# Kernel optimization log

Measured on AMD Instinct MI355X. Metric: run time of the kernel, lower is better.

The kernel has to match this reference:

```python
import jax, jax.numpy as jnp
import numpy as np

DIM = 1024
DFF = 4096
B, L = 4, 4096


def _lin_init(key, din, dout):
    k1, k2 = jax.random.split(key)
    bound = 1.0 / np.sqrt(din)
    w = jax.random.uniform(k1, (din, dout), jnp.float32, -bound, bound)
    b = jax.random.uniform(k2, (dout,), jnp.float32, -bound, bound)
    return w, b


def setup_inputs() -> dict:
    key = jax.random.key(0)
    ks = jax.random.split(key, 12)
    x = jax.random.normal(ks[0], (B, L, DIM), jnp.float32)
    hidden = jax.random.normal(ks[1], (B, DIM), jnp.float32)
    w_ln_z, b_ln_z = _lin_init(ks[2], DIM, DIM)
    w_dt, b_dt = _lin_init(ks[3], DIM, DIM)
    w_y, b_y = _lin_init(ks[4], DIM, DIM)
    w_yg, b_yg = _lin_init(ks[5], DIM, DIM)
    w_ff, b_ff = _lin_init(ks[6], DIM, DFF)
    w_ffg, b_ffg = _lin_init(ks[7], DIM, DFF)
    w_ffo, b_ffo = _lin_init(ks[8], DFF, DIM)
    g_sio = jnp.ones((DIM,), jnp.float32)
    g_ffn = jnp.ones((DIM,), jnp.float32)
    return dict(x=x, hidden=hidden, w_ln_z=w_ln_z, b_ln_z=b_ln_z, w_dt=w_dt,
                b_dt=b_dt, w_y=w_y, b_y=b_y, w_yg=w_yg, b_yg=b_yg,
                w_ff=w_ff, b_ff=b_ff, w_ffg=w_ffg, b_ffg=b_ffg,
                w_ffo=w_ffo, b_ffo=b_ffo, g_sio=g_sio, g_ffn=g_ffn)


def _rmsnorm(x, g, eps=1e-6):
    return x * jax.lax.rsqrt(jnp.mean(x * x, axis=-1, keepdims=True) + eps) * g


def reference(x, hidden, w_ln_z, b_ln_z, w_dt, b_dt, w_y, b_y, w_yg, b_yg,
              w_ff, b_ff, w_ffg, b_ffg, w_ffo, b_ffo, g_sio, g_ffn):
    silu = jax.nn.silu
    sp = jax.nn.softplus
    # --- SioConv branch ---
    residual = x
    xn = _rmsnorm(x, g_sio)
    dt = xn @ w_dt + b_dt
    ln_z = -sp(-(xn @ w_ln_z + b_ln_z))
    ln_da = -sp(-dt)           # log sigmoid(dt)
    ln_o_da = -sp(dt)          # log sigmoid(-dt)
    ln_o_da_cumsum = jnp.cumsum(ln_o_da, axis=1)
    lcse = jax.lax.cumlogsumexp(ln_z + ln_da - ln_o_da_cumsum, axis=1)
    h_inner = jnp.exp(lcse + ln_o_da_cumsum)                 # [B,L,D]
    h_cross = jnp.exp(ln_o_da_cumsum) * hidden[:, None, :]   # [B,L,D]
    h = h_inner + h_cross
    y = (h @ w_y + b_y) * silu(xn @ w_yg + b_yg)
    x = y + residual
    # --- FFN branch ---
    residual = x
    xn = _rmsnorm(x, g_ffn)
    ff = ((xn @ w_ff + b_ff) * silu(xn @ w_ffg + b_ffg)) @ w_ffo + b_ffo
    x = ff + residual
    return (x, h)
```

## Files before the change

kernel.cpp:

```cpp
#include <hip/hip_runtime.h>
#include <cstdint>
#include <cstddef>

using u16 = unsigned short;
using bf16x8 = __attribute__((ext_vector_type(8))) short;
using f32x4  = __attribute__((ext_vector_type(4))) float;

__device__ __forceinline__ u16 f2bf(float f) {
  unsigned u = __float_as_uint(f);
  u += 0x7fffu + ((u >> 16) & 1u);
  return (u16)(u >> 16);
}
__device__ __forceinline__ float bf2f(u16 h) {
  return __uint_as_float(((unsigned)h) << 16);
}

__device__ __forceinline__ void gload_lds16(const void* g, void* l) {
  auto gp = reinterpret_cast<const __attribute__((address_space(1))) char*>(
      reinterpret_cast<uintptr_t>(g));
  auto lp = reinterpret_cast<__attribute__((address_space(3))) char*>(
      reinterpret_cast<uintptr_t>(l));
  __builtin_amdgcn_global_load_lds(gp, lp, 16, 0, 0);
}

__global__ __launch_bounds__(256) void transpose_to_bf16(
    const float* __restrict__ W, u16* __restrict__ WT, int din, int dout) {
  __shared__ float tile[32][33];
  const int j0 = blockIdx.x * 32;
  const int i0 = blockIdx.y * 32;
  const int tx = threadIdx.x & 31;
  const int ty = threadIdx.x >> 5;
#pragma unroll
  for (int k = 0; k < 32; k += 8)
    tile[ty + k][tx] = W[(size_t)(i0 + ty + k) * dout + (j0 + tx)];
  __syncthreads();
#pragma unroll
  for (int k = 0; k < 32; k += 8)
    WT[(size_t)(j0 + ty + k) * din + (i0 + tx)] = f2bf(tile[tx][ty + k]);
}

__global__ __launch_bounds__(256) void rmsnorm_kernel(
    const float* __restrict__ x, const float* __restrict__ g, u16* __restrict__ xn) {
  const int row = blockIdx.x;
  const float4 v = ((const float4*)(x + (size_t)row * 1024))[threadIdx.x];
  float ss = v.x * v.x + v.y * v.y + v.z * v.z + v.w * v.w;
#pragma unroll
  for (int off = 32; off > 0; off >>= 1) ss += __shfl_down(ss, off, 64);
  __shared__ float red[4];
  if ((threadIdx.x & 63) == 0) red[threadIdx.x >> 6] = ss;
  __syncthreads();
  const float rs = rsqrtf((red[0] + red[1] + red[2] + red[3]) * (1.f / 1024.f) + 1e-6f);
  const float4 gv = ((const float4*)g)[threadIdx.x];
  ushort4 o;
  o.x = f2bf(v.x * rs * gv.x);
  o.y = f2bf(v.y * rs * gv.y);
  o.z = f2bf(v.z * rs * gv.z);
  o.w = f2bf(v.w * rs * gv.w);
  ((ushort4*)(xn + (size_t)row * 1024))[threadIdx.x] = o;
}

__global__ __launch_bounds__(256) void scan_pass1(
    const u16* __restrict__ dt, const u16* __restrict__ lnz,
    float* __restrict__ P, float* __restrict__ S) {
  const int blk = blockIdx.x;
  const int dblk = blk & 3;
  const int chunk = (blk >> 2) & 63;
  const int b = blk >> 8;
  const int d = dblk * 256 + threadIdx.x;
  const size_t base = ((size_t)b * 4096 + (size_t)chunk * 64) * 1024 + d;
  float p = 1.f, s = 0.f;
#pragma unroll 8
  for (int l = 0; l < 64; ++l) {
    const float dtv = bf2f(dt[base + (size_t)l * 1024]);
    const float zv = bf2f(lnz[base + (size_t)l * 1024]);
    const float a = 1.f / (1.f + __expf(dtv));
    const float zs = 1.f / (1.f + __expf(-zv));
    const float in = (1.f - a) * zs;
    p *= a;
    s = a * s + in;
  }
  const size_t o = ((size_t)b * 64 + chunk) * 1024 + d;
  P[o] = p;
  S[o] = s;
}

__global__ __launch_bounds__(256) void scan_pass2(
    const float* __restrict__ P, const float* __restrict__ S,
    const float* __restrict__ hidden, float* __restrict__ hin) {
  const int idx = blockIdx.x * 256 + threadIdx.x;
  const int b = idx >> 10, d = idx & 1023;
  float h = hidden[idx];
#pragma unroll 8
  for (int c = 0; c < 64; ++c) {
    const size_t o = ((size_t)b * 64 + c) * 1024 + d;
    hin[o] = h;
    h = P[o] * h + S[o];
  }
}

__global__ __launch_bounds__(256) void scan_pass3(
    const u16* __restrict__ dt, const u16* __restrict__ lnz,
    const float* __restrict__ hin, float* __restrict__ h_out, u16* __restrict__ hbf) {
  const int blk = blockIdx.x;
  const int dblk = blk & 3;
  const int chunk = (blk >> 2) & 63;
  const int b = blk >> 8;
  const int d = dblk * 256 + threadIdx.x;
  const size_t base = ((size_t)b * 4096 + (size_t)chunk * 64) * 1024 + d;
  float h = hin[((size_t)b * 64 + chunk) * 1024 + d];
#pragma unroll 4
  for (int l = 0; l < 64; ++l) {
    const float dtv = bf2f(dt[base + (size_t)l * 1024]);
    const float zv = bf2f(lnz[base + (size_t)l * 1024]);
    const float a = 1.f / (1.f + __expf(dtv));
    const float zs = 1.f / (1.f + __expf(-zv));
    h = a * h + (1.f - a) * zs;
    h_out[base + (size_t)l * 1024] = h;
    hbf[base + (size_t)l * 1024] = f2bf(h);
  }
}

template <int EPI>
__global__ __launch_bounds__(512, 4) void gemm256(
    const u16* __restrict__ A, const u16* __restrict__ B,
    const float* __restrict__ bias, const u16* __restrict__ gate,
    const float* __restrict__ resid, float* __restrict__ outF,
    u16* __restrict__ outH, u16* __restrict__ outH2, u16* __restrict__ outH3,
    int ntx, int N, int K) {
  constexpr int SLOT = 16384;
  const int tid = threadIdx.x;
  const int lane = tid & 63;
  const int wid = tid >> 6;
  const int wrow = wid >> 1;
  const int wcol = wid & 1;
  const int whalf = wrow >> 1;
  const int wsub  = wrow & 1;

  const int nwg = gridDim.x;
  int id = blockIdx.x;
  id = (id & 7) * (nwg >> 3) + (id >> 3);
  const int m0 = (id / ntx) * 256;
  const int n0 = (id % ntx) * 128;

  __shared__ __align__(16) char lds[5 * SLOT];

  f32x4 acc[4][4];
#pragma unroll
  for (int m = 0; m < 4; ++m)
#pragma unroll
    for (int n = 0; n < 4; ++n) acc[m][n] = (f32x4){0.f, 0.f, 0.f, 0.f};

  bf16x8 aR[2];
  bf16x8 bR[4][2];

  int aOff[4], bOff[4];
  {
    const int lq = (lane >> 4) << 4;
#pragma unroll
    for (int m = 0; m < 4; ++m) {
      const int hr = wsub * 64 + m * 16 + (lane & 15);
      aOff[m] = hr * 128 + (lq ^ ((hr & 7) << 4));
    }
#pragma unroll
    for (int n = 0; n < 4; ++n) {
      const int hr = wcol * 64 + n * 16 + (lane & 15);
      bOff[n] = hr * 128 + (lq ^ ((hr & 7) << 4));
    }
  }

  const int row0 = tid >> 3;
  const int kb0  = ((tid & 7) * 16) ^ ((row0 & 7) << 4);
  const size_t dRow = (size_t)128 * K;
  const char* pA0 = (const char*)A + (size_t)(m0 + row0) * K * 2 + kb0;
  const char* pA1 = pA0 + (size_t)256 * K;
  const char* pB  = (const char*)B + (size_t)(n0 + row0) * K * 2 + kb0;
  const int ldst = tid * 16;

#define STAGE(PTR, SB)                                                        \
  {                                                                           \
    gload_lds16(PTR, lds + (SB) + ldst);                                      \
    gload_lds16(PTR + dRow, lds + (SB) + ldst + 8192);                        \
    PTR += 128;                                                               \
  }

#define READA(SAB, Q)                                                         \
  {                                                                           \
    const int _o = aOff[Q];                                                   \
    aR[0] = *(const bf16x8*)(lds + (SAB) + _o);                               \
    aR[1] = *(const bf16x8*)(lds + (SAB) + (_o ^ 64));                        \
  }

#define READB(SBB)                                                            \
  _Pragma("unroll") for (int n = 0; n < 4; ++n) {                             \
    const int _o = bOff[n];                                                   \
    bR[n][0] = *(const bf16x8*)(lds + (SBB) + _o);                            \
    bR[n][1] = *(const bf16x8*)(lds + (SBB) + (_o ^ 64));                     \
  }

#define MMAQ(Q)                                                               \
  __builtin_amdgcn_s_setprio(1);                                              \
  _Pragma("unroll") for (int n = 0; n < 4; ++n)                               \
  _Pragma("unroll") for (int k = 0; k < 2; ++k)                               \
      acc[Q][n] = __builtin_amdgcn_mfma_f32_16x16x32_bf16(                    \
          aR[k], bR[n][k], acc[Q][n], 0, 0, 0);                               \
  __builtin_amdgcn_s_setprio(0);

  const int NT = K >> 6;

  STAGE(pB,  0 * SLOT);
  STAGE(pA0, 1 * SLOT);
  STAGE(pA1, 2 * SLOT);
  asm volatile("s_waitcnt vmcnt(0)" ::: "memory");
  __builtin_amdgcn_s_barrier();

  int iB = 0;

  for (int t = 0; t < NT; ++t) {
    int ib1 = iB + 1 + whalf; if (ib1 >= 5) ib1 -= 5;
    const int sAb = __builtin_amdgcn_readfirstlane(ib1 * SLOT);
    const int sBb = __builtin_amdgcn_readfirstlane(iB * SLOT);
    int i0s = iB + 3; if (i0s >= 5) i0s -= 5;
    int i1s = iB + 4; if (i1s >= 5) i1s -= 5;
    const int s0 = i0s * SLOT, s1 = i1s * SLOT, s2 = iB * SLOT;
    const bool st = (t < NT - 1);
    READB(sBb);
    READA(sAb, 0);
    if (st) STAGE(pB, s0);
    MMAQ(0);
    READA(sAb, 1);
    if (st) STAGE(pA0, s1);
    MMAQ(1);
    READA(sAb, 2);
    MMAQ(2);
    __builtin_amdgcn_s_barrier();
    READA(sAb, 3);
    if (st) STAGE(pA1, s2);
    MMAQ(3);
    asm volatile("s_waitcnt vmcnt(0)" ::: "memory");
    __builtin_amdgcn_s_barrier();
    iB += 3; if (iB >= 5) iB -= 5;
  }

#pragma unroll
  for (int m = 0; m < 4; ++m) {
#pragma unroll
    for (int n = 0; n < 4; ++n) {
      const int col = n0 + wcol * 64 + n * 16 + (lane & 15);
#pragma unroll
      for (int j = 0; j < 4; ++j) {
        const int row = m0 + wrow * 64 + m * 16 + ((lane >> 4) << 2) + j;
        const float v = acc[m][n][j] + bias[col];
        if constexpr (EPI == 5) {
          const int rg = col >> 10;
          const size_t o = (size_t)row * 1024 + (col & 1023);
          if (rg == 0) outH[o] = f2bf(v);
          else if (rg == 1) outH2[o] = f2bf(v);
          else outH3[o] = f2bf(v);
        } else {
          const size_t o = (size_t)row * N + col;
          if constexpr (EPI == 2) {
            const float gt = bf2f(gate[o]);
            outF[o] = v * (gt / (1.f + __expf(-gt))) + resid[o];
          } else if constexpr (EPI == 6) {
            outH[o] = f2bf(v / (1.f + __expf(-v)));
          } else if constexpr (EPI == 7) {
            outH[o] = f2bf(v * bf2f(gate[o]));
          } else if constexpr (EPI == 4) {
            outF[o] = v + outF[o];
          }
        }
      }
    }
  }
#undef STAGE
#undef READA
#undef READB
#undef MMAQ
}

extern "C" void kernel_launch(void* const* d_in, const int* in_sizes, int n_in,
                              void* d_out, int out_size, void* d_ws, size_t ws_size,
                              hipStream_t stream) {
  const float* x      = (const float*)d_in[0];
  const float* hidden = (const float*)d_in[1];
  const float* w_ln_z = (const float*)d_in[2];
  const float* b_ln_z = (const float*)d_in[3];
  const float* w_dt   = (const float*)d_in[4];
  const float* b_dt   = (const float*)d_in[5];
  const float* w_y    = (const float*)d_in[6];
  const float* b_y    = (const float*)d_in[7];
  const float* w_yg   = (const float*)d_in[8];
  const float* b_yg   = (const float*)d_in[9];
  const float* w_ff   = (const float*)d_in[10];
  const float* b_ff   = (const float*)d_in[11];
  const float* w_ffg  = (const float*)d_in[12];
  const float* b_ffg  = (const float*)d_in[13];
  const float* w_ffo  = (const float*)d_in[14];
  const float* b_ffo  = (const float*)d_in[15];
  const float* g_sio  = (const float*)d_in[16];
  const float* g_ffn  = (const float*)d_in[17];

  char* ws = (char*)d_ws;
  const size_t MB = 1ull << 20;
  u16*   WT_cat = (u16*)(ws + 0 * MB);
  u16*   WT_y   = (u16*)(ws + 8 * MB);
  u16*   WT_ff  = (u16*)(ws + 10 * MB);
  u16*   WT_ffg = (u16*)(ws + 18 * MB);
  u16*   WT_ffo = (u16*)(ws + 26 * MB);
  float* b_cat  = (float*)(ws + 34 * MB);
  u16*   xn     = (u16*)(ws + 36 * MB);
  u16*   dt16   = (u16*)(ws + 68 * MB);
  u16*   lnzb   = (u16*)(ws + 100 * MB);
  u16*   ygb    = (u16*)(ws + 132 * MB);
  u16*   hbf    = (u16*)(ws + 164 * MB);
  float* Pc     = (float*)(ws + 196 * MB);
  float* Sc     = (float*)(ws + 197 * MB);
  float* hin    = (float*)(ws + 198 * MB);
  u16*   gs     = (u16*)(ws + 68 * MB);

  float* x_out = (float*)d_out;
  float* h_out = (float*)d_out + (size_t)4 * 4096 * 1024;

  const int M = 16384, D = 1024, F = 4096;
  const dim3 tb(256);

  transpose_to_bf16<<<dim3(32, 32), tb, 0, stream>>>(w_dt, WT_cat, D, D);
  transpose_to_bf16<<<dim3(32, 32), tb, 0, stream>>>(w_ln_z, WT_cat + 1024 * 1024, D, D);
  transpose_to_bf16<<<dim3(32, 32), tb, 0, stream>>>(w_yg, WT_cat + 2 * 1024 * 1024, D, D);
  transpose_to_bf16<<<dim3(32, 32), tb, 0, stream>>>(w_y, WT_y, D, D);
  transpose_to_bf16<<<dim3(128, 32), tb, 0, stream>>>(w_ff, WT_ff, D, F);
  transpose_to_bf16<<<dim3(128, 32), tb, 0, stream>>>(w_ffg, WT_ffg, D, F);
  transpose_to_bf16<<<dim3(32, 128), tb, 0, stream>>>(w_ffo, WT_ffo, F, D);
  (void)hipMemcpyAsync(b_cat, b_dt, D * 4, hipMemcpyDeviceToDevice, stream);
  (void)hipMemcpyAsync(b_cat + 1024, b_ln_z, D * 4, hipMemcpyDeviceToDevice, stream);
  (void)hipMemcpyAsync(b_cat + 2048, b_yg, D * 4, hipMemcpyDeviceToDevice, stream);

  rmsnorm_kernel<<<M, tb, 0, stream>>>(x, g_sio, xn);

  gemm256<5><<<dim3(64 * 24), 512, 0, stream>>>(xn, WT_cat, b_cat, nullptr, nullptr,
                                                nullptr, dt16, lnzb, ygb, 24, 3072, D);

  scan_pass1<<<1024, tb, 0, stream>>>(dt16, lnzb, Pc, Sc);
  scan_pass2<<<16, tb, 0, stream>>>(Pc, Sc, hidden, hin);
  scan_pass3<<<1024, tb, 0, stream>>>(dt16, lnzb, hin, h_out, hbf);

  gemm256<2><<<dim3(64 * 8), 512, 0, stream>>>(hbf, WT_y, b_y, ygb, x,
                                               x_out, nullptr, nullptr, nullptr, 8, D, D);

  rmsnorm_kernel<<<M, tb, 0, stream>>>(x_out, g_ffn, xn);

  gemm256<6><<<dim3(64 * 32), 512, 0, stream>>>(xn, WT_ffg, b_ffg, nullptr, nullptr,
                                                nullptr, gs, nullptr, nullptr, 32, F, D);
  gemm256<7><<<dim3(64 * 32), 512, 0, stream>>>(xn, WT_ff, b_ff, gs, nullptr,
                                                nullptr, gs, nullptr, nullptr, 32, F, D);
  gemm256<4><<<dim3(64 * 8), 512, 0, stream>>>(gs, WT_ffo, b_ffo, nullptr, nullptr,
                                               x_out, nullptr, nullptr, nullptr, 8, D, F);
}
```

Measured before the change: 745.9 us.

## Fuse FFN up and gate GEMMs into one dual-B kernel with SwiGLU epilogue

Restructures the GEMM so that each block stages two 64-row B tiles and keeps two accumulator sets. For the FFN this computes the up and gate projections in one pass and applies silu(gate)*up in the epilogue. That removes the separate gate kernel, the bf16 round-trip of the gate tensor through global memory, and one full read of the A operand. Other GEMMs use the same kernel, with the two halves covering adjacent 64-column slices. The gated path now has 64-column tiles per projection, which doubles the grid and halves A reuse per B column.

```diff
diff --git a/kernel.cpp b/kernel.cpp
--- a/kernel.cpp
+++ b/kernel.cpp
@@ -121,13 +121,15 @@
 }
 
 template <int EPI>
-__global__ __launch_bounds__(512, 4) void gemm256(
-    const u16* __restrict__ A, const u16* __restrict__ B,
-    const float* __restrict__ bias, const u16* __restrict__ gate,
-    const float* __restrict__ resid, float* __restrict__ outF,
-    u16* __restrict__ outH, u16* __restrict__ outH2, u16* __restrict__ outH3,
+__global__ __launch_bounds__(512, 4) void gemm_pair(
+    const u16* __restrict__ A, const u16* __restrict__ B1, const u16* __restrict__ B2,
+    const float* __restrict__ biasA, const float* __restrict__ biasB,
+    const u16* __restrict__ gate, const float* __restrict__ resid,
+    float* __restrict__ outF, u16* __restrict__ outH,
+    u16* __restrict__ outH2, u16* __restrict__ outH3,
     int ntx, int N, int K) {
   constexpr int SLOT = 16384;
+  constexpr bool GATED = (EPI == 3);
   const int tid = threadIdx.x;
   const int lane = tid & 63;
   const int wid = tid >> 6;
@@ -140,32 +142,29 @@
   int id = blockIdx.x;
   id = (id & 7) * (nwg >> 3) + (id >> 3);
   const int m0 = (id / ntx) * 256;
-  const int n0 = (id % ntx) * 128;
+  const int n0 = (id % ntx) * (GATED ? 64 : 128);
 
   __shared__ __align__(16) char lds[5 * SLOT];
 
-  f32x4 acc[4][4];
+  f32x4 acc1[4][2], acc2[4][2];
 #pragma unroll
   for (int m = 0; m < 4; ++m)
 #pragma unroll
-    for (int n = 0; n < 4; ++n) acc[m][n] = (f32x4){0.f, 0.f, 0.f, 0.f};
+    for (int n = 0; n < 2; ++n) {
+      acc1[m][n] = (f32x4){0.f, 0.f, 0.f, 0.f};
+      acc2[m][n] = (f32x4){0.f, 0.f, 0.f, 0.f};
+    }
 
   bf16x8 aR[2];
-  bf16x8 bR[4][2];
-
-  int aOff[4], bOff[4];
+  bf16x8 b1R[2][2], b2R[2][2];
+
+  int aOff0, bOff0;
   {
     const int lq = (lane >> 4) << 4;
-#pragma unroll
-    for (int m = 0; m < 4; ++m) {
-      const int hr = wsub * 64 + m * 16 + (lane & 15);
-      aOff[m] = hr * 128 + (lq ^ ((hr & 7) << 4));
-    }
-#pragma unroll
-    for (int n = 0; n < 4; ++n) {
-      const int hr = wcol * 64 + n * 16 + (lane & 15);
-      bOff[n] = hr * 128 + (lq ^ ((hr & 7) << 4));
-    }
+    const int ha = wsub * 64 + (lane & 15);
+    aOff0 = ha * 128 + (lq ^ ((ha & 7) << 4));
+    const int hb = wcol * 32 + (lane & 15);
+    bOff0 = hb * 128 + (lq ^ ((hb & 7) << 4));
   }
 
   const int row0 = tid >> 3;
@@ -173,43 +172,56 @@
   const size_t dRow = (size_t)128 * K;
   const char* pA0 = (const char*)A + (size_t)(m0 + row0) * K * 2 + kb0;
   const char* pA1 = pA0 + (size_t)256 * K;
-  const char* pB  = (const char*)B + (size_t)(n0 + row0) * K * 2 + kb0;
+  const char* pB1 = (const char*)B1 + (size_t)(n0 + row0) * K * 2 + kb0;
+  const char* pB2 = (const char*)B2 +
+                    (size_t)((GATED ? n0 : n0 + 64) + row0) * K * 2 + kb0;
   const int ldst = tid * 16;
 
-#define STAGE(PTR, SB)                                                        \
+#define STAGEA(PTR, SB)                                                       \
   {                                                                           \
     gload_lds16(PTR, lds + (SB) + ldst);                                      \
     gload_lds16(PTR + dRow, lds + (SB) + ldst + 8192);                        \
     PTR += 128;                                                               \
   }
+#define STAGEB(PTR, SB, OFF)                                                  \
+  {                                                                           \
+    gload_lds16(PTR, lds + (SB) + (OFF) + ldst);                              \
+    PTR += 128;                                                               \
+  }
 
 #define READA(SAB, Q)                                                         \
   {                                                                           \
-    const int _o = aOff[Q];                                                   \
+    const int _o = aOff0 + (Q) * 2048;                                        \
     aR[0] = *(const bf16x8*)(lds + (SAB) + _o);                               \
     aR[1] = *(const bf16x8*)(lds + (SAB) + (_o ^ 64));                        \
   }
 
-#define READB(SBB)                                                            \
-  _Pragma("unroll") for (int n = 0; n < 4; ++n) {                             \
-    const int _o = bOff[n];                                                   \
-    bR[n][0] = *(const bf16x8*)(lds + (SBB) + _o);                            \
-    bR[n][1] = *(const bf16x8*)(lds + (SBB) + (_o ^ 64));                     \
-  }
-
-#define MMAQ(Q)                                                               \
+#define READBD(SBB)                                                           \
+  _Pragma("unroll") for (int n = 0; n < 2; ++n) {                             \
+    const int _o = bOff0 + n * 2048;                                          \
+    b1R[n][0] = *(const bf16x8*)(lds + (SBB) + _o);                           \
+    b1R[n][1] = *(const bf16x8*)(lds + (SBB) + (_o ^ 64));                    \
+    b2R[n][0] = *(const bf16x8*)(lds + (SBB) + 8192 + _o);                    \
+    b2R[n][1] = *(const bf16x8*)(lds + (SBB) + 8192 + (_o ^ 64));             \
+  }
+
+#define MMAD(Q)                                                               \
   __builtin_amdgcn_s_setprio(1);                                              \
-  _Pragma("unroll") for (int n = 0; n < 4; ++n)                               \
-  _Pragma("unroll") for (int k = 0; k < 2; ++k)                               \
-      acc[Q][n] = __builtin_amdgcn_mfma_f32_16x16x32_bf16(                    \
-          aR[k], bR[n][k], acc[Q][n], 0, 0, 0);                               \
+  _Pragma("unroll") for (int n = 0; n < 2; ++n)                               \
+  _Pragma("unroll") for (int k = 0; k < 2; ++k) {                             \
+    acc1[Q][n] = __builtin_amdgcn_mfma_f32_16x16x32_bf16(                     \
+        aR[k], b1R[n][k], acc1[Q][n], 0, 0, 0);                               \
+    acc2[Q][n] = __builtin_amdgcn_mfma_f32_16x16x32_bf16(                     \
+        aR[k], b2R[n][k], acc2[Q][n], 0, 0, 0);                               \
+  }                                                                           \
   __builtin_amdgcn_s_setprio(0);
 
   const int NT = K >> 6;
 
-  STAGE(pB,  0 * SLOT);
-  STAGE(pA0, 1 * SLOT);
-  STAGE(pA1, 2 * SLOT);
+  STAGEB(pB1, 0 * SLOT, 0);
+  STAGEB(pB2, 0 * SLOT, 8192);
+  STAGEA(pA0, 1 * SLOT);
+  STAGEA(pA1, 2 * SLOT);
   asm volatile("s_waitcnt vmcnt(0)" ::: "memory");
   __builtin_amdgcn_s_barrier();
 
@@ -223,19 +235,22 @@
     int i1s = iB + 4; if (i1s >= 5) i1s -= 5;
     const int s0 = i0s * SLOT, s1 = i1s * SLOT, s2 = iB * SLOT;
     const bool st = (t < NT - 1);
-    READB(sBb);
+    READBD(sBb);
     READA(sAb, 0);
-    if (st) STAGE(pB, s0);
-    MMAQ(0);
+    if (st) {
+      STAGEB(pB1, s0, 0);
+      STAGEB(pB2, s0, 8192);
+    }
+    MMAD(0);
     READA(sAb, 1);
-    if (st) STAGE(pA0, s1);
-    MMAQ(1);
+    if (st) STAGEA(pA0, s1);
+    MMAD(1);
     READA(sAb, 2);
-    MMAQ(2);
+    MMAD(2);
     __builtin_amdgcn_s_barrier();
     READA(sAb, 3);
-    if (st) STAGE(pA1, s2);
-    MMAQ(3);
+    if (st) STAGEA(pA1, s2);
+    MMAD(3);
     asm volatile("s_waitcnt vmcnt(0)" ::: "memory");
     __builtin_amdgcn_s_barrier();
     iB += 3; if (iB >= 5) iB -= 5;
@@ -244,38 +259,45 @@
 #pragma unroll
   for (int m = 0; m < 4; ++m) {
 #pragma unroll
-    for (int n = 0; n < 4; ++n) {
-      const int col = n0 + wcol * 64 + n * 16 + (lane & 15);
+    for (int n = 0; n < 2; ++n) {
 #pragma unroll
       for (int j = 0; j < 4; ++j) {
         const int row = m0 + wrow * 64 + m * 16 + ((lane >> 4) << 2) + j;
-        const float v = acc[m][n][j] + bias[col];
-        if constexpr (EPI == 5) {
-          const int rg = col >> 10;
-          const size_t o = (size_t)row * 1024 + (col & 1023);
-          if (rg == 0) outH[o] = f2bf(v);
-          else if (rg == 1) outH2[o] = f2bf(v);
-          else outH3[o] = f2bf(v);
+        if constexpr (GATED) {
+          const int col = n0 + wcol * 32 + n * 16 + (lane & 15);
+          const float v1 = acc1[m][n][j] + biasA[col];
+          const float v2 = acc2[m][n][j] + biasB[col];
+          outH[(size_t)row * N + col] = f2bf(v1 * (v2 / (1.f + __expf(-v2))));
         } else {
-          const size_t o = (size_t)row * N + col;
-          if constexpr (EPI == 2) {
-            const float gt = bf2f(gate[o]);
-            outF[o] = v * (gt / (1.f + __expf(-gt))) + resid[o];
-          } else if constexpr (EPI == 6) {
-            outH[o] = f2bf(v / (1.f + __expf(-v)));
-          } else if constexpr (EPI == 7) {
-            outH[o] = f2bf(v * bf2f(gate[o]));
-          } else if constexpr (EPI == 4) {
-            outF[o] = v + outF[o];
+#pragma unroll
+          for (int s = 0; s < 2; ++s) {
+            const int col = n0 + s * 64 + wcol * 32 + n * 16 + (lane & 15);
+            const float v = (s == 0 ? acc1[m][n][j] : acc2[m][n][j]) + biasA[col];
+            if constexpr (EPI == 5) {
+              const int rg = col >> 10;
+              const size_t o = (size_t)row * 1024 + (col & 1023);
+              if (rg == 0) outH[o] = f2bf(v);
+              else if (rg == 1) outH2[o] = f2bf(v);
+              else outH3[o] = f2bf(v);
+            } else {
+              const size_t o = (size_t)row * N + col;
+              if constexpr (EPI == 2) {
+                const float gt = bf2f(gate[o]);
+                outF[o] = v * (gt / (1.f + __expf(-gt))) + resid[o];
+              } else if constexpr (EPI == 4) {
+                outF[o] = v + outF[o];
+              }
+            }
           }
         }
       }
     }
   }
-#undef STAGE
+#undef STAGEA
+#undef STAGEB
 #undef READA
-#undef READB
-#undef MMAQ
+#undef READBD
+#undef MMAD
 }
 
 extern "C" void kernel_launch(void* const* d_in, const int* in_sizes, int n_in,
@@ -337,22 +359,25 @@
 
   rmsnorm_kernel<<<M, tb, 0, stream>>>(x, g_sio, xn);
 
-  gemm256<5><<<dim3(64 * 24), 512, 0, stream>>>(xn, WT_cat, b_cat, nullptr, nullptr,
-                                                nullptr, dt16, lnzb, ygb, 24, 3072, D);
+  gemm_pair<5><<<dim3(64 * 24), 512, 0, stream>>>(
+      xn, WT_cat, WT_cat, b_cat, nullptr, nullptr, nullptr,
+      nullptr, dt16, lnzb, ygb, 24, 3072, D);
 
   scan_pass1<<<1024, tb, 0, stream>>>(dt16, lnzb, Pc, Sc);
   scan_pass2<<<16, tb, 0, stream>>>(Pc, Sc, hidden, hin);
   scan_pass3<<<1024, tb, 0, stream>>>(dt16, lnzb, hin, h_out, hbf);
 
-  gemm256<2><<<dim3(64 * 8), 512, 0, stream>>>(hbf, WT_y, b_y, ygb, x,
-                                               x_out, nullptr, nullptr, nullptr, 8, D, D);
+  gemm_pair<2><<<dim3(64 * 8), 512, 0, stream>>>(
+      hbf, WT_y, WT_y, b_y, nullptr, ygb, x,
+      x_out, nullptr, nullptr, nullptr, 8, D, D);
 
   rmsnorm_kernel<<<M, tb, 0, stream>>>(x_out, g_ffn, xn);
 
-  gemm256<6><<<dim3(64 * 32), 512, 0, stream>>>(xn, WT_ffg, b_ffg, nullptr, nullptr,
-                                                nullptr, gs, nullptr, nullptr, 32, F, D);
-  gemm256<7><<<dim3(64 * 32), 512, 0, stream>>>(xn, WT_ff, b_ff, gs, nullptr,
-                                                nullptr, gs, nullptr, nullptr, 32, F, D);
-  gemm256<4><<<dim3(64 * 8), 512, 0, stream>>>(gs, WT_ffo, b_ffo, nullptr, nullptr,
-                                               x_out, nullptr, nullptr, nullptr, 8, D, F);
-}
+  gemm_pair<3><<<dim3(64 * 64), 512, 0, stream>>>(
+      xn, WT_ff, WT_ffg, b_ff, b_ffg, nullptr, nullptr,
+      nullptr, gs, nullptr, nullptr, 64, F, D);
+
+  gemm_pair<4><<<dim3(64 * 8), 512, 0, stream>>>(
+      gs, WT_ffo, WT_ffo, b_ffo, nullptr, nullptr, nullptr,
+      x_out, nullptr, nullptr, nullptr, 8, D, F);
+}
```

Result: faster. 716.8 us (-3.9%).
